# Kernel tuning notes

Hardware: AMD Instinct MI355X
Metric: run time of the kernel (lower is better)

Reference implementation:

```python
import jax, jax.numpy as jnp
import numpy as np

N_HEAD = 16
N_KV_HEAD = 8
HEAD_DIM = 64
EPS_NORM = 1e-6


def _rms_norm(x):
    # F.rms_norm without learned weight
    return x * jax.lax.rsqrt(jnp.mean(x * x, axis=-1, keepdims=True) + EPS_NORM)


def _apply_rotary_emb(x, cos, sin):
    # x: [B, T, H, D]; cos/sin: [T, 1, D/2] (broadcast over B and H)
    d = x.shape[-1] // 2
    x1, x2 = x[..., :d], x[..., d:]
    return jnp.concatenate([x1 * cos + x2 * sin, -x1 * sin + x2 * cos], axis=-1)


def setup_inputs() -> dict:
    key = jax.random.key(0)
    ks = jax.random.split(key, 8)
    B, T, C = 2, 2048, 1024
    return {
        "x": jax.random.normal(ks[0], (B, T, C), jnp.float32),
        "cos": jax.random.uniform(ks[1], (T, 1, HEAD_DIM // 2), jnp.float32),
        "sin": jax.random.uniform(ks[2], (T, 1, HEAD_DIM // 2), jnp.float32),
        "Wq": jax.random.normal(ks[3], (N_HEAD * HEAD_DIM, C), jnp.float32) * 0.02,
        "Wk": jax.random.normal(ks[4], (N_KV_HEAD * HEAD_DIM, C), jnp.float32) * 0.02,
        "Wv": jax.random.normal(ks[5], (N_KV_HEAD * HEAD_DIM, C), jnp.float32) * 0.02,
        "Wproj": jax.random.normal(ks[6], (C, C), jnp.float32) * 0.02,
        "w_braid": jax.random.normal(ks[7], (HEAD_DIM,), jnp.float32),
    }


def reference(x, cos, sin, Wq, Wk, Wv, Wproj, w_braid):
    B, T, C = x.shape
    q = (x @ Wq.T).reshape(B, T, N_HEAD, HEAD_DIM)
    k = (x @ Wk.T).reshape(B, T, N_KV_HEAD, HEAD_DIM)
    v = (x @ Wv.T).reshape(B, T, N_KV_HEAD, HEAD_DIM)
    q = _rms_norm(_apply_rotary_emb(q, cos, sin))
    k = _rms_norm(_apply_rotary_emb(k, cos, sin))
    # [B, H, T, D]
    q = q.transpose(0, 2, 1, 3)
    k = k.transpose(0, 2, 1, 3)
    v = v.transpose(0, 2, 1, 3)
    rep = N_HEAD // N_KV_HEAD
    k = jnp.repeat(k, rep, axis=1)  # GQA repeat_kv_heads
    v = jnp.repeat(v, rep, axis=1)
    # rank-1 outer-sum score: s_q[i] + s_k[j]
    s_q = jnp.einsum("bhtd,d->bht", q, w_braid)
    s_k = jnp.einsum("bhsd,d->bhs", k, w_braid)
    scores = s_q[..., :, None] + s_k[..., None, :]  # [B, H, T, T]
    causal = jnp.arange(T)[:, None] >= jnp.arange(T)[None, :]
    scores = jnp.where(causal, scores, -jnp.inf)
    attn = jax.nn.sigmoid(scores)  # non-softmax gating
    y = jnp.einsum("bhts,bhsd->bhtd", attn, v)
    y = y / (T ** 0.5 + 1e-6)
    y = y.transpose(0, 2, 1, 3).reshape(B, T, C)
    return y @ Wproj.T
```

## Files before the change

### kernel.cpp

```cpp
#include <hip/hip_runtime.h>

#define BATCH   2
#define T_LEN   2048
#define C_DIM   1024
#define NH      16
#define NKV     8
#define HD      64

typedef unsigned short u16;
typedef __attribute__((ext_vector_type(8))) short short8;
typedef __attribute__((ext_vector_type(4))) float floatx4;

__device__ __forceinline__ u16 f2bf(float f) {
    union { float f; unsigned u; } v; v.f = f;
    unsigned r = v.u + 0x7FFF + ((v.u >> 16) & 1);
    return (u16)(r >> 16);
}

__device__ __forceinline__ void gload_lds16(const u16* g, u16* l) {
    __builtin_amdgcn_global_load_lds(
        (const __attribute__((address_space(1))) void*)g,
        (__attribute__((address_space(3))) void*)l, 16, 0, 0);
}

__global__ __launch_bounds__(256)
void cvt_all(const float* __restrict__ x, const float* __restrict__ Wq,
             const float* __restrict__ Wk, const float* __restrict__ Wv,
             const float* __restrict__ Wp, u16* __restrict__ xb,
             u16* __restrict__ Wqkvb, u16* __restrict__ Wpb) {
    const int blk = blockIdx.x;
    const float* src; u16* dst; long off;
    if (blk < 4096)      { src = x;  dst = xb;              off = (long)blk * 1024; }
    else if (blk < 5120) { src = Wq; dst = Wqkvb;           off = (long)(blk - 4096) * 1024; }
    else if (blk < 5632) { src = Wk; dst = Wqkvb + 1048576; off = (long)(blk - 5120) * 1024; }
    else if (blk < 6144) { src = Wv; dst = Wqkvb + 1572864; off = (long)(blk - 5632) * 1024; }
    else                 { src = Wp; dst = Wpb;             off = (long)(blk - 6144) * 1024; }
    const long i = off + (long)threadIdx.x * 4;
    const float4 f = *(const float4*)&src[i];
    ushort4 o;
    o.x = f2bf(f.x); o.y = f2bf(f.y); o.z = f2bf(f.z); o.w = f2bf(f.w);
    *(ushort4*)&dst[i] = o;
}

__global__ __launch_bounds__(256)
void gemm_qkv(const u16* __restrict__ A, const u16* __restrict__ B,
              u16* __restrict__ Vt, float* __restrict__ esq,
              float* __restrict__ esk, const float* __restrict__ cosb,
              const float* __restrict__ sinb, const float* __restrict__ wb) {
    const int K = 1024;
    __shared__ u16 As[2][128 * 64];
    __shared__ u16 Bs[2][128 * 64];
    const int tid    = threadIdx.x;
    const int lane   = tid & 63;
    const int wave   = tid >> 6;
    const int row_in = lane & 15;
    const int quad   = lane >> 4;
    const int rw     = (wave & 1) * 64;
    const int cw     = (wave >> 1) * 64;
    const int bi   = blockIdx.x;
    const int xcd  = bi & 7;
    const int bj   = bi >> 3;
    const int row0 = (bj >> 1) * 128;
    const int col0 = (xcd * 2 + (bj & 1)) * 128;

    floatx4 acc[4][4] = {};

    const int n    = row_in;
    const int xa   = n & 7;

    const int sl_r[4]  = { (0*256+tid)>>3, (1*256+tid)>>3, (2*256+tid)>>3, (3*256+tid)>>3 };
    const int sl_kc[4] = { ((0*256+tid)&7)^(sl_r[0]&7), ((1*256+tid)&7)^(sl_r[1]&7),
                           ((2*256+tid)&7)^(sl_r[2]&7), ((3*256+tid)&7)^(sl_r[3]&7) };

    #pragma unroll
    for (int c = 0; c < 4; ++c) {
        const int l = c * 256 + tid;
        gload_lds16(A + (size_t)(row0 + sl_r[c]) * K + sl_kc[c] * 8, &As[0][(size_t)l * 8]);
        gload_lds16(B + (size_t)(col0 + sl_r[c]) * K + sl_kc[c] * 8, &Bs[0][(size_t)l * 8]);
    }
    __syncthreads();

    int cur = 0;
    for (int k0 = 0; k0 < K; k0 += 64) {
        if (k0 + 64 < K) {
            const int kn = k0 + 64;
            #pragma unroll
            for (int c = 0; c < 4; ++c) {
                const int l = c * 256 + tid;
                gload_lds16(A + (size_t)(row0 + sl_r[c]) * K + kn + sl_kc[c] * 8, &As[cur ^ 1][(size_t)l * 8]);
                gload_lds16(B + (size_t)(col0 + sl_r[c]) * K + kn + sl_kc[c] * 8, &Bs[cur ^ 1][(size_t)l * 8]);
            }
        }
        #pragma unroll
        for (int kk = 0; kk < 2; ++kk) {
            const int co = ((kk * 4 + quad) ^ xa) * 8;
            short8 af[4], bf_[4];
            #pragma unroll
            for (int i = 0; i < 4; ++i)
                af[i] = *(const short8*)&As[cur][(rw + 16 * i + n) * 64 + co];
            #pragma unroll
            for (int j = 0; j < 4; ++j)
                bf_[j] = *(const short8*)&Bs[cur][(cw + 16 * j + n) * 64 + co];
            #pragma unroll
            for (int i = 0; i < 4; ++i)
                #pragma unroll
                for (int j = 0; j < 4; ++j)
                    acc[i][j] = __builtin_amdgcn_mfma_f32_16x16x32_bf16(af[i], bf_[j], acc[i][j], 0, 0, 0);
        }
        __syncthreads();
        cur ^= 1;
    }

    const int cw_g = col0 + cw;
    const int rw_g = row0 + rw;
    const int ch   = cw_g >> 6;

    if (ch < 24) {
        const float w0 = wb[n], w1 = wb[16 + n], w2 = wb[32 + n], w3 = wb[48 + n];
        #pragma unroll
        for (int i = 0; i < 4; ++i)
            #pragma unroll
            for (int r = 0; r < 4; ++r) {
                const int grow = rw_g + 16 * i + quad * 4 + r;
                const int t = grow & 2047;
                const int b = grow >> 11;
                const float c0 = cosb[t * 32 + n];
                const float c1 = cosb[t * 32 + 16 + n];
                const float s0 = sinb[t * 32 + n];
                const float s1 = sinb[t * 32 + 16 + n];
                const float x0 = acc[i][0][r], x1 = acc[i][1][r];
                const float x2 = acc[i][2][r], x3 = acc[i][3][r];
                const float r0 = fmaf(x0, c0,  x2 * s0);
                const float r1 = fmaf(x1, c1,  x3 * s1);
                const float r2 = fmaf(x2, c0, -x0 * s0);
                const float r3 = fmaf(x3, c1, -x1 * s1);
                float ss = r0 * r0 + r1 * r1 + r2 * r2 + r3 * r3;
                float dt = r0 * w0 + r1 * w1 + r2 * w2 + r3 * w3;
                #pragma unroll
                for (int m = 1; m < 16; m <<= 1) {
                    ss += __shfl_xor(ss, m, 64);
                    dt += __shfl_xor(dt, m, 64);
                }
                const float val = dt * rsqrtf(ss * (1.0f / 64.0f) + 1e-6f);
                const float e = __expf(-fminf(fmaxf(val, -44.0f), 44.0f));
                if (n == 0) {
                    if (ch < 16) esq[((size_t)b * NH + ch) * T_LEN + t] = e;
                    else         esk[((size_t)b * NKV + ch - 16) * T_LEN + t] = e;
                }
            }
    } else {
        const int vcol = cw_g - 1536;
        const int b    = rw_g >> 11;
        const int tb   = (rw_g & 2047) + quad * 4;
        #pragma unroll
        for (int j = 0; j < 4; ++j) {
            const int dg  = vcol + 16 * j + n;
            const int kvh = dg >> 6;
            const int din = dg & 63;
            u16* dstp = Vt + ((size_t)(b * NKV + kvh) * 64 + din) * T_LEN;
            #pragma unroll
            for (int i = 0; i < 4; ++i) {
                ushort4 o;
                o.x = f2bf(acc[i][j][0]);
                o.y = f2bf(acc[i][j][1]);
                o.z = f2bf(acc[i][j][2]);
                o.w = f2bf(acc[i][j][3]);
                *(ushort4*)&dstp[tb + 16 * i] = o;
            }
        }
    }
}

__global__ __launch_bounds__(512)
void braid_attn(const float* __restrict__ esq, const float* __restrict__ esk,
                const u16* __restrict__ Vt, u16* __restrict__ yb) {
    __shared__ u16 Vd[2][2][4096];
    __shared__ float eskl[2][128];
    __shared__ float red[4096];

    const int bi   = blockIdx.x;
    const int g    = (bi & 7) * 2 + ((bi >> 8) & 1);
    const int wnd  = (bi >> 3) & 31;
    const int b    = g >> 3;
    const int kvh  = g & 7;
    const int h    = kvh * 2 + (wnd >> 4);
    const int p    = wnd & 15;
    const int bh   = b * 16 + h;
    const int tid  = threadIdx.x;
    const int lane = tid & 63;
    const int wave = tid >> 6;
    const int sg   = wave >> 2;
    const int w4   = wave & 3;
    const int n    = lane & 15;
    const int quad = lane >> 4;
    const int row  = w4 * 16 + n;

    const float* esq_p = esq + (size_t)bh * T_LEN;
    const float* esk_p = esk + ((size_t)b * NKV + kvh) * T_LEN;
    const u16*   vt_b  = Vt + ((size_t)b * NKV + kvh) * 64 * T_LEN;
    const float  inv   = (float)(1.0 / (45.254833995939045 + 1e-6));

    const int st_r  = tid >> 3;
    const int st_so = ((tid & 7) ^ (st_r & 7)) << 3;

    for (int ph = 0; ph < 2; ++ph) {
        const int t0 = (ph ? p : (31 - p)) * 64;
        const float a = esq_p[t0 + row];
        const int send = t0 + 64;
        floatx4 acc[4] = {};

        gload_lds16(vt_b + (size_t)st_r * T_LEN + st_so, &Vd[0][0][(size_t)tid * 8]);
        if (64 < send)
            gload_lds16(vt_b + (size_t)st_r * T_LEN + 64 + st_so, &Vd[0][1][(size_t)tid * 8]);
        if (tid < 128 && (tid < 64 || 64 < send))
            eskl[0][tid] = esk_p[tid];
        __syncthreads();

        int cur = 0;
        for (int s0 = 0; s0 < send; s0 += 128) {
            const int s0n = s0 + 128;
            if (s0n < send) {
                gload_lds16(vt_b + (size_t)st_r * T_LEN + s0n + st_so, &Vd[cur ^ 1][0][(size_t)tid * 8]);
                if (s0n + 64 < send)
                    gload_lds16(vt_b + (size_t)st_r * T_LEN + s0n + 64 + st_so, &Vd[cur ^ 1][1][(size_t)tid * 8]);
                if (tid < 128 && (tid < 64 || s0n + 64 < send))
                    eskl[cur ^ 1][tid] = esk_p[s0n + tid];
            }

            const int s0g = s0 + sg * 64;
            if (s0g < send) {
                const bool diag = (s0g == t0);
                #pragma unroll
                for (int kk = 0; kk < 2; ++kk) {
                    const float* eb = &eskl[cur][sg * 64 + kk * 32 + quad * 8];
                    const float4 e0 = *(const float4*)eb;
                    const float4 e1 = *(const float4*)(eb + 4);
                    const float ev[8] = {e0.x, e0.y, e0.z, e0.w, e1.x, e1.y, e1.z, e1.w};
                    union { unsigned u[4]; short8 s8; } af;
                    #pragma unroll
                    for (int jj = 0; jj < 4; ++jj) {
                        float r0 = __builtin_amdgcn_rcpf(fmaf(ev[2 * jj],     a, 1.0f));
                        float r1 = __builtin_amdgcn_rcpf(fmaf(ev[2 * jj + 1], a, 1.0f));
                        if (diag) {
                            const int s_ = kk * 32 + quad * 8 + 2 * jj;
                            if (s_     > row) r0 = 0.0f;
                            if (s_ + 1 > row) r1 = 0.0f;
                        }
                        af.u[jj] = __builtin_amdgcn_perm(__float_as_uint(r1),
                                                         __float_as_uint(r0), 0x07060302u);
                    }
                    #pragma unroll
                    for (int j = 0; j < 4; ++j) {
                        const short8 bfr = *(const short8*)
                            &Vd[cur][sg][(16 * j + n) * 64 + (((kk * 4 + quad) ^ (n & 7)) << 3)];
                        acc[j] = __builtin_amdgcn_mfma_f32_16x16x32_bf16(af.s8, bfr, acc[j], 0, 0, 0);
                    }
                }
            }
            __syncthreads();
            cur ^= 1;
        }

        if (sg == 1) {
            #pragma unroll
            for (int j = 0; j < 4; ++j)
                #pragma unroll
                for (int r = 0; r < 4; ++r)
                    red[(j * 4 + r) * 256 + w4 * 64 + lane] = acc[j][r];
        }
        __syncthreads();
        if (sg == 0) {
            #pragma unroll
            for (int j = 0; j < 4; ++j)
                #pragma unroll
                for (int r = 0; r < 4; ++r) {
                    const float o = acc[j][r] + red[(j * 4 + r) * 256 + w4 * 64 + lane];
                    const int t = t0 + w4 * 16 + quad * 4 + r;
                    yb[((size_t)b * T_LEN + t) * C_DIM + h * HD + 16 * j + n] = f2bf(o * inv);
                }
        }
    }
}

__global__ __launch_bounds__(256)
void gemm_proj(const u16* __restrict__ A, const u16* __restrict__ B,
               float* __restrict__ C, int M, int N, int K) {
    __shared__ u16 As[2][128 * 64];
    __shared__ u16 Bs[2][64 * 64];
    const int tid    = threadIdx.x;
    const int lane   = tid & 63;
    const int wave   = tid >> 6;
    const int row_in = lane & 15;
    const int quad   = lane >> 4;
    const int rw     = (wave & 1) * 64;
    const int cw     = (wave >> 1) * 32;
    const int bi   = blockIdx.x;
    const int xcd  = bi & 7;
    const int bj   = bi >> 3;
    const int row0 = (bj >> 1) * 128;
    const int col0 = (xcd * 2 + (bj & 1)) * 64;

    floatx4 acc[4][2] = {};

    const int n  = row_in;
    const int xa = n & 7;

    #pragma unroll
    for (int c = 0; c < 4; ++c) {
        const int l  = c * 256 + tid;
        const int r  = l >> 3;
        const int kc = (l & 7) ^ (r & 7);
        gload_lds16(A + (size_t)(row0 + r) * K + kc * 8, &As[0][(size_t)l * 8]);
    }
    #pragma unroll
    for (int c = 0; c < 2; ++c) {
        const int l  = c * 256 + tid;
        const int r  = l >> 3;
        const int kc = (l & 7) ^ (r & 7);
        gload_lds16(B + (size_t)(col0 + r) * K + kc * 8, &Bs[0][(size_t)l * 8]);
    }
    __syncthreads();

    int cur = 0;
    for (int k0 = 0; k0 < K; k0 += 64) {
        if (k0 + 64 < K) {
            const int kn = k0 + 64;
            #pragma unroll
            for (int c = 0; c < 4; ++c) {
                const int l  = c * 256 + tid;
                const int r  = l >> 3;
                const int kc = (l & 7) ^ (r & 7);
                gload_lds16(A + (size_t)(row0 + r) * K + kn + kc * 8, &As[cur ^ 1][(size_t)l * 8]);
            }
            #pragma unroll
            for (int c = 0; c < 2; ++c) {
                const int l  = c * 256 + tid;
                const int r  = l >> 3;
                const int kc = (l & 7) ^ (r & 7);
                gload_lds16(B + (size_t)(col0 + r) * K + kn + kc * 8, &Bs[cur ^ 1][(size_t)l * 8]);
            }
        }
        #pragma unroll
        for (int kk = 0; kk < 2; ++kk) {
            const int co = ((kk * 4 + quad) ^ xa) * 8;
            short8 af[4], bf_[2];
            #pragma unroll
            for (int i = 0; i < 4; ++i)
                af[i] = *(const short8*)&As[cur][(rw + 16 * i + n) * 64 + co];
            #pragma unroll
            for (int j = 0; j < 2; ++j)
                bf_[j] = *(const short8*)&Bs[cur][(cw + 16 * j + n) * 64 + co];
            #pragma unroll
            for (int i = 0; i < 4; ++i)
                #pragma unroll
                for (int j = 0; j < 2; ++j)
                    acc[i][j] = __builtin_amdgcn_mfma_f32_16x16x32_bf16(af[i], bf_[j], acc[i][j], 0, 0, 0);
        }
        __syncthreads();
        cur ^= 1;
    }

    #pragma unroll
    for (int i = 0; i < 4; ++i)
        #pragma unroll
        for (int j = 0; j < 2; ++j)
            #pragma unroll
            for (int r = 0; r < 4; ++r)
                C[(size_t)(row0 + rw + 16 * i + quad * 4 + r) * N + col0 + cw + 16 * j + row_in]
                    = acc[i][j][r];
}

extern "C" void kernel_launch(void* const* d_in, const int* in_sizes, int n_in,
                              void* d_out, int out_size, void* d_ws, size_t ws_size,
                              hipStream_t stream) {
    const float* x     = (const float*)d_in[0];
    const float* cosb  = (const float*)d_in[1];
    const float* sinb  = (const float*)d_in[2];
    const float* Wq    = (const float*)d_in[3];
    const float* Wk    = (const float*)d_in[4];
    const float* Wv    = (const float*)d_in[5];
    const float* Wproj = (const float*)d_in[6];
    const float* wb    = (const float*)d_in[7];
    float* out = (float*)d_out;

    char* w = (char*)d_ws;
    u16* xb     = (u16*)w;  w += (size_t)4096 * 1024 * 2;
    u16* Wqkvb  = (u16*)w;  w += (size_t)2048 * 1024 * 2;
    u16* Wpb    = (u16*)w;  w += (size_t)1024 * 1024 * 2;
    u16* yb     = (u16*)w;  w += (size_t)4096 * 1024 * 2;
    u16* VtB    = (u16*)w;  w += (size_t)BATCH * NKV * 64 * T_LEN * 2;
    float* esq  = (float*)w; w += (size_t)BATCH * NH * T_LEN * 4;
    float* esk  = (float*)w; w += (size_t)BATCH * NKV * T_LEN * 4;

    dim3 blk(256);
    cvt_all<<<7168, blk, 0, stream>>>(x, Wq, Wk, Wv, Wproj, xb, Wqkvb, Wpb);
    gemm_qkv<<<512, blk, 0, stream>>>(xb, Wqkvb, VtB, esq, esk, cosb, sinb, wb);
    braid_attn<<<512, dim3(512), 0, stream>>>(esq, esk, VtB, yb);
    gemm_proj<<<512, blk, 0, stream>>>(yb, Wpb, out, 4096, 1024, 1024);
}
```

Measured before the change: 153.6 us.

## Deepen GEMM LDS pipeline to prefetch two K-tiles ahead with explicit waitcnts

Restructures the QKV and projection GEMM main loops so two K-tiles are in flight. Each iteration first loads all fragments for the current tile from LDS into registers, then hits a barrier, then issues the global-to-LDS loads for tile kt+2 into that same buffer. The MFMAs run while those loads proceed, and partial vmcnt waits replace full __syncthreads. This aims to hide global load latency behind compute, at the cost of more registers for fragments and fragile hand-counted waitcnt and sched_barrier logic.

After: 148.0 us, median of 2. 3.7% less time.

```diff
diff --git a/kernel.cpp b/kernel.cpp
--- a/kernel.cpp
+++ b/kernel.cpp
@@ -22,6 +22,10 @@
         (const __attribute__((address_space(1))) void*)g,
         (__attribute__((address_space(3))) void*)l, 16, 0, 0);
 }
+
+#define SBAR   __builtin_amdgcn_s_barrier()
+#define SCHED0 __builtin_amdgcn_sched_barrier(0)
+#define WAIT_LGKM0 asm volatile("s_waitcnt lgkmcnt(0)" ::: "memory")
 
 __global__ __launch_bounds__(256)
 void cvt_all(const float* __restrict__ x, const float* __restrict__ Wq,
@@ -47,7 +51,8 @@
               u16* __restrict__ Vt, float* __restrict__ esq,
               float* __restrict__ esk, const float* __restrict__ cosb,
               const float* __restrict__ sinb, const float* __restrict__ wb) {
-    const int K = 1024;
+    const int K  = 1024;
+    const int NK = 16;
     __shared__ u16 As[2][128 * 64];
     __shared__ u16 Bs[2][128 * 64];
     const int tid    = threadIdx.x;
@@ -75,39 +80,59 @@
     #pragma unroll
     for (int c = 0; c < 4; ++c) {
         const int l = c * 256 + tid;
-        gload_lds16(A + (size_t)(row0 + sl_r[c]) * K + sl_kc[c] * 8, &As[0][(size_t)l * 8]);
-        gload_lds16(B + (size_t)(col0 + sl_r[c]) * K + sl_kc[c] * 8, &Bs[0][(size_t)l * 8]);
-    }
-    __syncthreads();
+        gload_lds16(A + (size_t)(row0 + sl_r[c]) * K + 0  + sl_kc[c] * 8, &As[0][(size_t)l * 8]);
+        gload_lds16(B + (size_t)(col0 + sl_r[c]) * K + 0  + sl_kc[c] * 8, &Bs[0][(size_t)l * 8]);
+    }
+    #pragma unroll
+    for (int c = 0; c < 4; ++c) {
+        const int l = c * 256 + tid;
+        gload_lds16(A + (size_t)(row0 + sl_r[c]) * K + 64 + sl_kc[c] * 8, &As[1][(size_t)l * 8]);
+        gload_lds16(B + (size_t)(col0 + sl_r[c]) * K + 64 + sl_kc[c] * 8, &Bs[1][(size_t)l * 8]);
+    }
+    asm volatile("s_waitcnt vmcnt(8)" ::: "memory");
+    SBAR;
+    SCHED0;
 
     int cur = 0;
-    for (int k0 = 0; k0 < K; k0 += 64) {
-        if (k0 + 64 < K) {
-            const int kn = k0 + 64;
+    for (int kt = 0; kt < NK; ++kt) {
+        short8 af[2][4], bf_[2][4];
+        #pragma unroll
+        for (int kk = 0; kk < 2; ++kk) {
+            const int co = ((kk * 4 + quad) ^ xa) * 8;
+            #pragma unroll
+            for (int i = 0; i < 4; ++i)
+                af[kk][i] = *(const short8*)&As[cur][(rw + 16 * i + n) * 64 + co];
+            #pragma unroll
+            for (int j = 0; j < 4; ++j)
+                bf_[kk][j] = *(const short8*)&Bs[cur][(cw + 16 * j + n) * 64 + co];
+        }
+        WAIT_LGKM0;
+        SCHED0;
+        SBAR;
+        SCHED0;
+
+        if (kt + 2 < NK) {
+            const int kn = (kt + 2) * 64;
             #pragma unroll
             for (int c = 0; c < 4; ++c) {
                 const int l = c * 256 + tid;
-                gload_lds16(A + (size_t)(row0 + sl_r[c]) * K + kn + sl_kc[c] * 8, &As[cur ^ 1][(size_t)l * 8]);
-                gload_lds16(B + (size_t)(col0 + sl_r[c]) * K + kn + sl_kc[c] * 8, &Bs[cur ^ 1][(size_t)l * 8]);
+                gload_lds16(A + (size_t)(row0 + sl_r[c]) * K + kn + sl_kc[c] * 8, &As[cur][(size_t)l * 8]);
+                gload_lds16(B + (size_t)(col0 + sl_r[c]) * K + kn + sl_kc[c] * 8, &Bs[cur][(size_t)l * 8]);
             }
         }
-        #pragma unroll
-        for (int kk = 0; kk < 2; ++kk) {
-            const int co = ((kk * 4 + quad) ^ xa) * 8;
-            short8 af[4], bf_[4];
+
+        #pragma unroll
+        for (int kk = 0; kk < 2; ++kk)
             #pragma unroll
             for (int i = 0; i < 4; ++i)
-                af[i] = *(const short8*)&As[cur][(rw + 16 * i + n) * 64 + co];
-            #pragma unroll
-            for (int j = 0; j < 4; ++j)
-                bf_[j] = *(const short8*)&Bs[cur][(cw + 16 * j + n) * 64 + co];
-            #pragma unroll
-            for (int i = 0; i < 4; ++i)
                 #pragma unroll
                 for (int j = 0; j < 4; ++j)
-                    acc[i][j] = __builtin_amdgcn_mfma_f32_16x16x32_bf16(af[i], bf_[j], acc[i][j], 0, 0, 0);
-        }
-        __syncthreads();
+                    acc[i][j] = __builtin_amdgcn_mfma_f32_16x16x32_bf16(af[kk][i], bf_[kk][j], acc[i][j], 0, 0, 0);
+
+        if (kt < NK - 2) { asm volatile("s_waitcnt vmcnt(8)" ::: "memory"); }
+        else             { asm volatile("s_waitcnt vmcnt(0)" ::: "memory"); }
+        SBAR;
+        SCHED0;
         cur ^= 1;
     }
 
@@ -285,6 +310,7 @@
 __global__ __launch_bounds__(256)
 void gemm_proj(const u16* __restrict__ A, const u16* __restrict__ B,
                float* __restrict__ C, int M, int N, int K) {
+    const int NK = 16;
     __shared__ u16 As[2][128 * 64];
     __shared__ u16 Bs[2][64 * 64];
     const int tid    = threadIdx.x;
@@ -305,58 +331,68 @@
     const int n  = row_in;
     const int xa = n & 7;
 
-    #pragma unroll
-    for (int c = 0; c < 4; ++c) {
-        const int l  = c * 256 + tid;
-        const int r  = l >> 3;
-        const int kc = (l & 7) ^ (r & 7);
-        gload_lds16(A + (size_t)(row0 + r) * K + kc * 8, &As[0][(size_t)l * 8]);
-    }
-    #pragma unroll
-    for (int c = 0; c < 2; ++c) {
-        const int l  = c * 256 + tid;
-        const int r  = l >> 3;
-        const int kc = (l & 7) ^ (r & 7);
-        gload_lds16(B + (size_t)(col0 + r) * K + kc * 8, &Bs[0][(size_t)l * 8]);
-    }
-    __syncthreads();
+    const int sa_r[4]  = { (0*256+tid)>>3, (1*256+tid)>>3, (2*256+tid)>>3, (3*256+tid)>>3 };
+    const int sa_kc[4] = { ((0*256+tid)&7)^(sa_r[0]&7), ((1*256+tid)&7)^(sa_r[1]&7),
+                           ((2*256+tid)&7)^(sa_r[2]&7), ((3*256+tid)&7)^(sa_r[3]&7) };
+    const int sb_r[2]  = { (0*256+tid)>>3, (1*256+tid)>>3 };
+    const int sb_kc[2] = { ((0*256+tid)&7)^(sb_r[0]&7), ((1*256+tid)&7)^(sb_r[1]&7) };
+
+    #pragma unroll
+    for (int c = 0; c < 4; ++c)
+        gload_lds16(A + (size_t)(row0 + sa_r[c]) * K + 0 + sa_kc[c] * 8, &As[0][(size_t)(c*256+tid) * 8]);
+    #pragma unroll
+    for (int c = 0; c < 2; ++c)
+        gload_lds16(B + (size_t)(col0 + sb_r[c]) * K + 0 + sb_kc[c] * 8, &Bs[0][(size_t)(c*256+tid) * 8]);
+    #pragma unroll
+    for (int c = 0; c < 4; ++c)
+        gload_lds16(A + (size_t)(row0 + sa_r[c]) * K + 64 + sa_kc[c] * 8, &As[1][(size_t)(c*256+tid) * 8]);
+    #pragma unroll
+    for (int c = 0; c < 2; ++c)
+        gload_lds16(B + (size_t)(col0 + sb_r[c]) * K + 64 + sb_kc[c] * 8, &Bs[1][(size_t)(c*256+tid) * 8]);
+    asm volatile("s_waitcnt vmcnt(6)" ::: "memory");
+    SBAR;
+    SCHED0;
 
     int cur = 0;
-    for (int k0 = 0; k0 < K; k0 += 64) {
-        if (k0 + 64 < K) {
-            const int kn = k0 + 64;
-            #pragma unroll
-            for (int c = 0; c < 4; ++c) {
-                const int l  = c * 256 + tid;
-                const int r  = l >> 3;
-                const int kc = (l & 7) ^ (r & 7);
-                gload_lds16(A + (size_t)(row0 + r) * K + kn + kc * 8, &As[cur ^ 1][(size_t)l * 8]);
-            }
-            #pragma unroll
-            for (int c = 0; c < 2; ++c) {
-                const int l  = c * 256 + tid;
-                const int r  = l >> 3;
-                const int kc = (l & 7) ^ (r & 7);
-                gload_lds16(B + (size_t)(col0 + r) * K + kn + kc * 8, &Bs[cur ^ 1][(size_t)l * 8]);
-            }
-        }
+    for (int kt = 0; kt < NK; ++kt) {
+        short8 af[2][4], bf_[2][2];
         #pragma unroll
         for (int kk = 0; kk < 2; ++kk) {
             const int co = ((kk * 4 + quad) ^ xa) * 8;
-            short8 af[4], bf_[2];
             #pragma unroll
             for (int i = 0; i < 4; ++i)
-                af[i] = *(const short8*)&As[cur][(rw + 16 * i + n) * 64 + co];
+                af[kk][i] = *(const short8*)&As[cur][(rw + 16 * i + n) * 64 + co];
             #pragma unroll
             for (int j = 0; j < 2; ++j)
-                bf_[j] = *(const short8*)&Bs[cur][(cw + 16 * j + n) * 64 + co];
+                bf_[kk][j] = *(const short8*)&Bs[cur][(cw + 16 * j + n) * 64 + co];
+        }
+        WAIT_LGKM0;
+        SCHED0;
+        SBAR;
+        SCHED0;
+
+        if (kt + 2 < NK) {
+            const int kn = (kt + 2) * 64;
+            #pragma unroll
+            for (int c = 0; c < 4; ++c)
+                gload_lds16(A + (size_t)(row0 + sa_r[c]) * K + kn + sa_kc[c] * 8, &As[cur][(size_t)(c*256+tid) * 8]);
+            #pragma unroll
+            for (int c = 0; c < 2; ++c)
+                gload_lds16(B + (size_t)(col0 + sb_r[c]) * K + kn + sb_kc[c] * 8, &Bs[cur][(size_t)(c*256+tid) * 8]);
+        }
+
+        #pragma unroll
+        for (int kk = 0; kk < 2; ++kk)
             #pragma unroll
             for (int i = 0; i < 4; ++i)
                 #pragma unroll
                 for (int j = 0; j < 2; ++j)
-                    acc[i][j] = __builtin_amdgcn_mfma_f32_16x16x32_bf16(af[i], bf_[j], acc[i][j], 0, 0, 0);
-        }
-        __syncthreads();
+                    acc[i][j] = __builtin_amdgcn_mfma_f32_16x16x32_bf16(af[kk][i], bf_[kk][j], acc[i][j], 0, 0, 0);
+
+        if (kt < NK - 2) { asm volatile("s_waitcnt vmcnt(6)" ::: "memory"); }
+        else             { asm volatile("s_waitcnt vmcnt(0)" ::: "memory"); }
+        SBAR;
+        SCHED0;
         cur ^= 1;
     }
 
```
